# Performance work log

Measured on AMD Instinct MI355X. Metric: run time of the kernel, lower is better.

## Reference

```python
import jax, jax.numpy as jnp
import numpy as np

N_HEADS = 16
N_EMBD = 1024

def setup_inputs() -> dict:
    key = jax.random.key(0)
    k1, k2, k3, k4, k5 = jax.random.split(key, 5)
    B, T, C = 4, 2048, N_EMBD
    x = jax.random.normal(k1, (B, T, C), dtype=jnp.float32)
    # Linear weights stored as [in, out] (equivalent math to torch's x @ W.T + b)
    W_attn = jax.random.normal(k2, (C, 3 * C), dtype=jnp.float32) * 0.02
    b_attn = jax.random.normal(k3, (3 * C,), dtype=jnp.float32) * 0.02
    W_proj = jax.random.normal(k4, (C, C), dtype=jnp.float32) * 0.02
    b_proj = jax.random.normal(k5, (C,), dtype=jnp.float32) * 0.02
    return {"x": x, "W_attn": W_attn, "b_attn": b_attn, "W_proj": W_proj, "b_proj": b_proj}

def reference(x, W_attn, b_attn, W_proj, b_proj):
    B, T, C = x.shape
    H = N_HEADS
    D = C // H
    scale = 1.0 / jnp.sqrt(jnp.asarray(D, dtype=x.dtype))
    # fused QKV projection
    qkv = x @ W_attn + b_attn                      # [B, T, 3C]
    q, k, v = jnp.split(qkv, 3, axis=-1)           # each [B, T, C]
    q = q.reshape(B, T, H, D)
    k = k.reshape(B, T, H, D)
    v = v.reshape(B, T, H, D)
    # non-causal SDPA
    scores = jnp.einsum('bqhd,bkhd->bhqk', q, k) * scale  # [B, H, T, T]
    attn = jax.nn.softmax(scores, axis=-1)
    y = jnp.einsum('bhqk,bkhd->bqhd', attn, v)     # [B, T, H, D]
    y = y.reshape(B, T, C)
    return y @ W_proj + b_proj
```

## Files before the change

### kernel.cpp

```cpp
#include <hip/hip_runtime.h>

typedef short s16x8 __attribute__((ext_vector_type(8)));
typedef short s16x4 __attribute__((ext_vector_type(4)));
typedef float f32x4 __attribute__((ext_vector_type(4)));
typedef float f32x16 __attribute__((ext_vector_type(16)));

__device__ __forceinline__ unsigned short f2bf(float f) {
  unsigned u = __float_as_uint(f);
  u += 0x7fffu + ((u >> 16) & 1u);
  return (unsigned short)(u >> 16);
}
__device__ __forceinline__ float bf2f(unsigned short h) {
  return __uint_as_float(((unsigned)h) << 16);
}

#define GLOAD_LDS16(g, l)                                          \
  __builtin_amdgcn_global_load_lds(                                \
      (const __attribute__((address_space(1))) void*)(g),          \
      (__attribute__((address_space(3))) void*)(l), 16, 0, 0)


__global__ __launch_bounds__(256) void cvt_x_bf16(const float* __restrict__ in,
                                                  unsigned short* __restrict__ out) {
  int i = (blockIdx.x * 256 + threadIdx.x) * 4;
  float4 v = *(const float4*)(in + i);
  ushort4 o;
  o.x = f2bf(v.x); o.y = f2bf(v.y); o.z = f2bf(v.z); o.w = f2bf(v.w);
  *(ushort4*)(out + i) = o;
}

__global__ __launch_bounds__(256) void transpose_w(const float* __restrict__ W,
                                                   unsigned short* __restrict__ Wt,
                                                   int R, int C) {
  __shared__ float tile[32][33];
  int c0 = blockIdx.x * 32, r0 = blockIdx.y * 32;
  int x = threadIdx.x, ty = threadIdx.y;
  for (int yy = ty; yy < 32; yy += 8)
    tile[yy][x] = W[(size_t)(r0 + yy) * C + c0 + x];
  __syncthreads();
  for (int yy = ty; yy < 32; yy += 8)
    Wt[(size_t)(c0 + yy) * R + r0 + x] = f2bf(tile[x][yy]);
}

__global__ __launch_bounds__(256) void transpose_v(const unsigned short* __restrict__ qkv,
                                                   unsigned short* __restrict__ vt) {
  __shared__ unsigned short TT[32][72];
  const int bh = blockIdx.y;
  const int t0 = blockIdx.x * 32;
  const int b = bh >> 4, h = bh & 15;
  const int t = threadIdx.x;
  {
    int row = t >> 3, c8 = (t & 7) * 8;
    const unsigned short* src =
        qkv + (size_t)(b * 2048 + t0 + row) * 3072 + 2048 + h * 64 + c8;
    *(uint4*)&TT[row][c8] = *(const uint4*)src;
  }
  __syncthreads();
  {
    int drow = t >> 2, tc8 = (t & 3) * 8;
    uint4 val;
    unsigned short* vp = (unsigned short*)&val;
    for (int j = 0; j < 8; j++) vp[j] = TT[tc8 + j][drow];
    *(uint4*)(vt + (size_t)(bh * 64 + drow) * 2048 + t0 + tc8) = val;
  }
}


template <bool OUT_BF16>
__global__ __launch_bounds__(256) void gemm_bt(const unsigned short* __restrict__ A,
                                               const unsigned short* __restrict__ Bt,
                                               const float* __restrict__ bias,
                                               void* __restrict__ Cout,
                                               int M, int N, int K) {
  __shared__ __align__(16) unsigned short As[2][128 * 32];
  __shared__ __align__(16) unsigned short Bs[2][128 * 32];

  const int tid  = threadIdx.x;
  const int lane = tid & 63;
  const int w    = tid >> 6;
  const int lm   = lane & 31;
  const int l5   = lane >> 5;
  const int wm   = (w >> 1) * 64;
  const int wn   = (w & 1) * 64;
  const int m0   = blockIdx.x * 128;
  const int n0   = blockIdx.y * 128;

  f32x16 acc[2][2];
  for (int i = 0; i < 2; i++)
    for (int j = 0; j < 2; j++)
      for (int r = 0; r < 16; r++) acc[i][j][r] = 0.f;

  const int srow = tid >> 2;
  const int scb  = (((tid & 3) ^ ((srow >> 1) & 3)) * 8);
  const unsigned short* Ap = A  + (size_t)(m0 + srow) * K + scb;
  const unsigned short* Bp = Bt + (size_t)(n0 + srow) * K + scb;

#define STAGE_G(bb, kk)                                                  \
  do {                                                                   \
    GLOAD_LDS16(Ap + (kk), &As[bb][w * 512]);                            \
    GLOAD_LDS16(Ap + (size_t)64 * K + (kk), &As[bb][2048 + w * 512]);    \
    GLOAD_LDS16(Bp + (kk), &Bs[bb][w * 512]);                            \
    GLOAD_LDS16(Bp + (size_t)64 * K + (kk), &Bs[bb][2048 + w * 512]);    \
  } while (0)

  const int rx = ((lm >> 1) & 3) << 4;

  STAGE_G(0, 0);
  int cur = 0;
  for (int kk = 0; kk < K; kk += 32) {
    __syncthreads();
    if (kk + 32 < K) STAGE_G(cur ^ 1, kk + 32);

    const char* Ab = (const char*)As[cur];
    const char* Bb = (const char*)Bs[cur];
    s16x8 af[2][2], bfr[2][2];
    for (int i = 0; i < 2; i++)
      for (int ks = 0; ks < 2; ks++)
        af[i][ks] = *(const s16x8*)(Ab + (wm + i * 32 + lm) * 64 +
                                    (((l5 * 16 + ks * 32)) ^ rx));
    for (int j = 0; j < 2; j++)
      for (int ks = 0; ks < 2; ks++)
        bfr[j][ks] = *(const s16x8*)(Bb + (wn + j * 32 + lm) * 64 +
                                     (((l5 * 16 + ks * 32)) ^ rx));
    for (int ks = 0; ks < 2; ks++)
      for (int i = 0; i < 2; i++)
        for (int j = 0; j < 2; j++)
          acc[i][j] = __builtin_amdgcn_mfma_f32_32x32x16_bf16(af[i][ks], bfr[j][ks],
                                                              acc[i][j], 0, 0, 0);
    cur ^= 1;
  }
#undef STAGE_G

  for (int j = 0; j < 2; j++) {
    int col = n0 + wn + j * 32 + lm;
    float bc = bias[col];
    for (int i = 0; i < 2; i++) {
      int rowb = m0 + wm + i * 32 + l5 * 4;
      for (int r = 0; r < 16; r++) {
        int row = rowb + (r & 3) + 8 * (r >> 2);
        float v = acc[i][j][r] + bc;
        if (OUT_BF16)
          ((unsigned short*)Cout)[(size_t)row * N + col] = f2bf(v);
        else
          ((float*)Cout)[(size_t)row * N + col] = v;
      }
    }
  }
}


__global__ __launch_bounds__(256, 4) void attn_flash(const unsigned short* __restrict__ qkv,
                                                     const unsigned short* __restrict__ vt,
                                                     unsigned short* __restrict__ y) {
  const int T = 2048, C3 = 3072;
  const int bh = blockIdx.x & 63;
  const int qt = blockIdx.x >> 6;
  const int b  = bh >> 4;
  const int h  = bh & 15;
  const int q0 = qt * 128;

  const int tid  = threadIdx.x;
  const int lane = tid & 63;
  const int w    = tid >> 6;
  const int lr   = lane & 15;
  const int quad = lane >> 4;

  __shared__ __align__(16) unsigned short Ks[2][64][64];
  __shared__ __align__(16) unsigned short Vs[2][64][64];

  s16x8 qf[2][2];
  const float QSC = 0.18033688f;
  for (int j = 0; j < 2; j++)
    for (int c = 0; c < 2; c++) {
      const unsigned short* qp =
          qkv + (size_t)(b * T + q0 + w * 32 + j * 16 + lr) * C3 + h * 64 + c * 32 + quad * 8;
      s16x8 t = *(const s16x8*)qp;
      s16x8 o;
      for (int e = 0; e < 8; e++)
        o[e] = (short)f2bf(bf2f((unsigned short)t[e]) * QSC);
      qf[j][c] = o;
    }

  s16x8 ones;
  for (int e = 0; e < 8; e++) ones[e] = (short)0x3F80;

  f32x4 O[2][4];
  f32x4 Lacc[2];
  for (int j = 0; j < 2; j++) {
    for (int dt = 0; dt < 4; dt++) O[j][dt] = f32x4{0.f, 0.f, 0.f, 0.f};
    Lacc[j] = f32x4{0.f, 0.f, 0.f, 0.f};
  }

  const int srow = tid >> 3;
  const int scol = (((tid & 7) ^ (srow & 7)) * 8);
  const int kperm = (((srow & 12) << 1) | ((srow >> 4) << 2) | (srow & 3));

  const unsigned short* kbase = qkv + (size_t)(b * T) * C3 + 1024 + (size_t)h * 64;
  const unsigned short* vbase = vt + (size_t)(bh * 64) * 2048;
  const unsigned short* kp0 = kbase + (size_t)(kperm)      * C3 + scol;
  const unsigned short* kp1 = kbase + (size_t)(32 + kperm) * C3 + scol;
  const unsigned short* vp0 = vbase + (size_t)(srow)      * 2048 + scol;
  const unsigned short* vp1 = vbase + (size_t)(srow + 32) * 2048 + scol;

#define STAGE_KV(bb, k0off)                                                  \
  do {                                                                       \
    GLOAD_LDS16(kp0 + (size_t)(k0off) * C3, &Ks[bb][w * 8][0]);              \
    GLOAD_LDS16(kp1 + (size_t)(k0off) * C3, &Ks[bb][w * 8 + 32][0]);         \
    GLOAD_LDS16(vp0 + (k0off), &Vs[bb][w * 8][0]);                           \
    GLOAD_LDS16(vp1 + (k0off), &Vs[bb][w * 8 + 32][0]);                      \
  } while (0)

  const int rswz = (lr & 7) << 4;

  STAGE_KV(0, 0);
  int cur = 0;
  for (int kt = 0; kt < 32; kt++) {
    __syncthreads();
    if (kt < 31) STAGE_KV(cur ^ 1, (kt + 1) * 64);

    const char* KsB = (const char*)&Ks[cur][0][0];
    const char* VsB = (const char*)&Vs[cur][0][0];

    for (int ch = 0; ch < 2; ch++) {
      const char* krowA = KsB + (ch * 32 + lr) * 128;
      const char* krowB = KsB + (ch * 32 + 16 + lr) * 128;
      s16x8 kA0 = *(const s16x8*)(krowA + ((quad * 16) ^ rswz));
      s16x8 kA1 = *(const s16x8*)(krowA + ((64 + quad * 16) ^ rswz));
      s16x8 kB0 = *(const s16x8*)(krowB + ((quad * 16) ^ rswz));
      s16x8 kB1 = *(const s16x8*)(krowB + ((64 + quad * 16) ^ rswz));
      s16x8 vf[4];
      for (int dt = 0; dt < 4; dt++)
        vf[dt] = *(const s16x8*)(VsB + (dt * 16 + lr) * 128 + ((ch * 64 + quad * 16) ^ rswz));

      for (int j = 0; j < 2; j++) {
        f32x4 Sa = f32x4{0.f, 0.f, 0.f, 0.f};
        f32x4 Sb = f32x4{0.f, 0.f, 0.f, 0.f};
        Sa = __builtin_amdgcn_mfma_f32_16x16x32_bf16(kA0, qf[j][0], Sa, 0, 0, 0);
        Sa = __builtin_amdgcn_mfma_f32_16x16x32_bf16(kA1, qf[j][1], Sa, 0, 0, 0);
        Sb = __builtin_amdgcn_mfma_f32_16x16x32_bf16(kB0, qf[j][0], Sb, 0, 0, 0);
        Sb = __builtin_amdgcn_mfma_f32_16x16x32_bf16(kB1, qf[j][1], Sb, 0, 0, 0);
        unsigned u0 = __float_as_uint(__builtin_amdgcn_exp2f(Sa[0])) + 0x8000u;
        unsigned u1 = __float_as_uint(__builtin_amdgcn_exp2f(Sa[1])) + 0x8000u;
        unsigned u2 = __float_as_uint(__builtin_amdgcn_exp2f(Sa[2])) + 0x8000u;
        unsigned u3 = __float_as_uint(__builtin_amdgcn_exp2f(Sa[3])) + 0x8000u;
        unsigned u4 = __float_as_uint(__builtin_amdgcn_exp2f(Sb[0])) + 0x8000u;
        unsigned u5 = __float_as_uint(__builtin_amdgcn_exp2f(Sb[1])) + 0x8000u;
        unsigned u6 = __float_as_uint(__builtin_amdgcn_exp2f(Sb[2])) + 0x8000u;
        unsigned u7 = __float_as_uint(__builtin_amdgcn_exp2f(Sb[3])) + 0x8000u;
        union { unsigned u[4]; s16x8 v; } pk;
        pk.u[0] = __builtin_amdgcn_perm(u1, u0, 0x07060302u);
        pk.u[1] = __builtin_amdgcn_perm(u3, u2, 0x07060302u);
        pk.u[2] = __builtin_amdgcn_perm(u5, u4, 0x07060302u);
        pk.u[3] = __builtin_amdgcn_perm(u7, u6, 0x07060302u);
        Lacc[j] = __builtin_amdgcn_mfma_f32_16x16x32_bf16(pk.v, ones, Lacc[j], 0, 0, 0);
        for (int dt = 0; dt < 4; dt++)
          O[j][dt] = __builtin_amdgcn_mfma_f32_16x16x32_bf16(pk.v, vf[dt], O[j][dt], 0, 0, 0);
      }
    }
    cur ^= 1;
  }
#undef STAGE_KV

  for (int j = 0; j < 2; j++) {
    for (int r = 0; r < 4; r++) {
      float inv = 1.f / Lacc[j][r];
      int row = b * T + q0 + w * 32 + j * 16 + quad * 4 + r;
      for (int dt = 0; dt < 4; dt++) {
        int col = h * 64 + dt * 16 + lr;
        y[(size_t)row * 1024 + col] = f2bf(O[j][dt][r] * inv);
      }
    }
  }
}


extern "C" void kernel_launch(void* const* d_in, const int* in_sizes, int n_in,
                              void* d_out, int out_size, void* d_ws, size_t ws_size,
                              hipStream_t stream) {
  const float* x  = (const float*)d_in[0];
  const float* Wa = (const float*)d_in[1];
  const float* ba = (const float*)d_in[2];
  const float* Wp = (const float*)d_in[3];
  const float* bp = (const float*)d_in[4];
  float* out = (float*)d_out;

  char* ws = (char*)d_ws;
  unsigned short* xb  = (unsigned short*)ws;
  unsigned short* Wat = (unsigned short*)(ws + 16777216);
  unsigned short* Wpt = (unsigned short*)(ws + 23068672);
  unsigned short* qkv = (unsigned short*)(ws + 25165824);
  unsigned short* vtr = (unsigned short*)(ws + 75497472);

  cvt_x_bf16<<<8192, 256, 0, stream>>>(x, xb);
  transpose_w<<<dim3(96, 32), dim3(32, 8), 0, stream>>>(Wa, Wat, 1024, 3072);
  transpose_w<<<dim3(32, 32), dim3(32, 8), 0, stream>>>(Wp, Wpt, 1024, 1024);

  gemm_bt<true><<<dim3(64, 24), 256, 0, stream>>>(xb, Wat, ba, qkv, 8192, 3072, 1024);

  transpose_v<<<dim3(64, 64), 256, 0, stream>>>(qkv, vtr);

  attn_flash<<<1024, 256, 0, stream>>>(qkv, vtr, xb);

  gemm_bt<false><<<dim3(64, 8), 256, 0, stream>>>(xb, Wpt, bp, out, 8192, 1024, 1024);
}
```

Baseline: 277.6 us.

## Fuse V transpose into QKV GEMM epilogue and unroll attention loop

The QKV GEMM now writes the V block directly in transposed [b,h,d,t] layout from its epilogue, which removes the separate transpose_v kernel and its extra read and write of V. The attention main loop is unrolled by two with fixed buffer indices and pointer increments. It also adds s_setprio around MFMA groups and uses the hardware packed bf16 convert in place of manual rounding. The V stores are now 8-byte strided writes along t, which may coalesce less well than the row-major writes they replace.

```diff
diff --git a/kernel.cpp b/kernel.cpp
--- a/kernel.cpp
+++ b/kernel.cpp
@@ -42,35 +42,13 @@
     Wt[(size_t)(c0 + yy) * R + r0 + x] = f2bf(tile[x][yy]);
 }
 
-__global__ __launch_bounds__(256) void transpose_v(const unsigned short* __restrict__ qkv,
-                                                   unsigned short* __restrict__ vt) {
-  __shared__ unsigned short TT[32][72];
-  const int bh = blockIdx.y;
-  const int t0 = blockIdx.x * 32;
-  const int b = bh >> 4, h = bh & 15;
-  const int t = threadIdx.x;
-  {
-    int row = t >> 3, c8 = (t & 7) * 8;
-    const unsigned short* src =
-        qkv + (size_t)(b * 2048 + t0 + row) * 3072 + 2048 + h * 64 + c8;
-    *(uint4*)&TT[row][c8] = *(const uint4*)src;
-  }
-  __syncthreads();
-  {
-    int drow = t >> 2, tc8 = (t & 3) * 8;
-    uint4 val;
-    unsigned short* vp = (unsigned short*)&val;
-    for (int j = 0; j < 8; j++) vp[j] = TT[tc8 + j][drow];
-    *(uint4*)(vt + (size_t)(bh * 64 + drow) * 2048 + t0 + tc8) = val;
-  }
-}
-
-
-template <bool OUT_BF16>
+
+template <int MODE>
 __global__ __launch_bounds__(256) void gemm_bt(const unsigned short* __restrict__ A,
                                                const unsigned short* __restrict__ Bt,
                                                const float* __restrict__ bias,
                                                void* __restrict__ Cout,
+                                               unsigned short* __restrict__ vtr,
                                                int M, int N, int K) {
   __shared__ __align__(16) unsigned short As[2][128 * 32];
   __shared__ __align__(16) unsigned short Bs[2][128 * 32];
@@ -131,18 +109,38 @@
   }
 #undef STAGE_G
 
-  for (int j = 0; j < 2; j++) {
-    int col = n0 + wn + j * 32 + lm;
-    float bc = bias[col];
-    for (int i = 0; i < 2; i++) {
-      int rowb = m0 + wm + i * 32 + l5 * 4;
-      for (int r = 0; r < 16; r++) {
-        int row = rowb + (r & 3) + 8 * (r >> 2);
-        float v = acc[i][j][r] + bc;
-        if (OUT_BF16)
-          ((unsigned short*)Cout)[(size_t)row * N + col] = f2bf(v);
-        else
-          ((float*)Cout)[(size_t)row * N + col] = v;
+  if (MODE == 1 && n0 >= 2048) {
+    const int bidx = m0 >> 11;
+    for (int j = 0; j < 2; j++) {
+      int col = n0 + wn + j * 32 + lm;
+      float bc = bias[col];
+      size_t vrow = (size_t)((bidx << 10) + (col - 2048)) * 2048;
+      for (int i = 0; i < 2; i++) {
+        int tb = (m0 & 2047) + wm + i * 32 + l5 * 4;
+        for (int g = 0; g < 4; g++) {
+          ushort4 o;
+          o.x = f2bf(acc[i][j][g * 4 + 0] + bc);
+          o.y = f2bf(acc[i][j][g * 4 + 1] + bc);
+          o.z = f2bf(acc[i][j][g * 4 + 2] + bc);
+          o.w = f2bf(acc[i][j][g * 4 + 3] + bc);
+          *(ushort4*)(vtr + vrow + tb + 8 * g) = o;
+        }
+      }
+    }
+  } else {
+    for (int j = 0; j < 2; j++) {
+      int col = n0 + wn + j * 32 + lm;
+      float bc = bias[col];
+      for (int i = 0; i < 2; i++) {
+        int rowb = m0 + wm + i * 32 + l5 * 4;
+        for (int r = 0; r < 16; r++) {
+          int row = rowb + (r & 3) + 8 * (r >> 2);
+          float v = acc[i][j][r] + bc;
+          if (MODE == 1)
+            ((unsigned short*)Cout)[(size_t)row * N + col] = f2bf(v);
+          else
+            ((float*)Cout)[(size_t)row * N + col] = v;
+        }
       }
     }
   }
@@ -202,64 +200,77 @@
   const unsigned short* vp0 = vbase + (size_t)(srow)      * 2048 + scol;
   const unsigned short* vp1 = vbase + (size_t)(srow + 32) * 2048 + scol;
 
-#define STAGE_KV(bb, k0off)                                                  \
+#define STAGE_KV(bb)                                                         \
   do {                                                                       \
-    GLOAD_LDS16(kp0 + (size_t)(k0off) * C3, &Ks[bb][w * 8][0]);              \
-    GLOAD_LDS16(kp1 + (size_t)(k0off) * C3, &Ks[bb][w * 8 + 32][0]);         \
-    GLOAD_LDS16(vp0 + (k0off), &Vs[bb][w * 8][0]);                           \
-    GLOAD_LDS16(vp1 + (k0off), &Vs[bb][w * 8 + 32][0]);                      \
+    GLOAD_LDS16(kp0, &Ks[bb][w * 8][0]);                                     \
+    GLOAD_LDS16(kp1, &Ks[bb][w * 8 + 32][0]);                                \
+    GLOAD_LDS16(vp0, &Vs[bb][w * 8][0]);                                     \
+    GLOAD_LDS16(vp1, &Vs[bb][w * 8 + 32][0]);                                \
+    kp0 += (size_t)64 * C3; kp1 += (size_t)64 * C3;                          \
+    vp0 += 64; vp1 += 64;                                                    \
   } while (0)
 
   const int rswz = (lr & 7) << 4;
 
-  STAGE_KV(0, 0);
-  int cur = 0;
-  for (int kt = 0; kt < 32; kt++) {
+#define COMPUTE(bb)                                                              \
+  do {                                                                           \
+    const char* KsB = (const char*)&Ks[bb][0][0];                                \
+    const char* VsB = (const char*)&Vs[bb][0][0];                                \
+    for (int ch = 0; ch < 2; ch++) {                                             \
+      const char* krowA = KsB + (ch * 32 + lr) * 128;                            \
+      const char* krowB = KsB + (ch * 32 + 16 + lr) * 128;                       \
+      s16x8 kA0 = *(const s16x8*)(krowA + ((quad * 16) ^ rswz));                 \
+      s16x8 kA1 = *(const s16x8*)(krowA + ((64 + quad * 16) ^ rswz));            \
+      s16x8 kB0 = *(const s16x8*)(krowB + ((quad * 16) ^ rswz));                 \
+      s16x8 kB1 = *(const s16x8*)(krowB + ((64 + quad * 16) ^ rswz));            \
+      s16x8 vf[4];                                                               \
+      for (int dt = 0; dt < 4; dt++)                                             \
+        vf[dt] = *(const s16x8*)(VsB + (dt * 16 + lr) * 128 +                    \
+                                 ((ch * 64 + quad * 16) ^ rswz));                \
+      for (int j = 0; j < 2; j++) {                                              \
+        f32x4 Sa = f32x4{0.f, 0.f, 0.f, 0.f};                                    \
+        f32x4 Sb = f32x4{0.f, 0.f, 0.f, 0.f};                                    \
+        __builtin_amdgcn_s_setprio(1);                                           \
+        Sa = __builtin_amdgcn_mfma_f32_16x16x32_bf16(kA0, qf[j][0], Sa, 0, 0, 0);\
+        Sa = __builtin_amdgcn_mfma_f32_16x16x32_bf16(kA1, qf[j][1], Sa, 0, 0, 0);\
+        Sb = __builtin_amdgcn_mfma_f32_16x16x32_bf16(kB0, qf[j][0], Sb, 0, 0, 0);\
+        Sb = __builtin_amdgcn_mfma_f32_16x16x32_bf16(kB1, qf[j][1], Sb, 0, 0, 0);\
+        __builtin_amdgcn_s_setprio(0);                                           \
+        float p0 = __builtin_amdgcn_exp2f(Sa[0]);                                \
+        float p1 = __builtin_amdgcn_exp2f(Sa[1]);                                \
+        float p2 = __builtin_amdgcn_exp2f(Sa[2]);                                \
+        float p3 = __builtin_amdgcn_exp2f(Sa[3]);                                \
+        float p4 = __builtin_amdgcn_exp2f(Sb[0]);                                \
+        float p5 = __builtin_amdgcn_exp2f(Sb[1]);                                \
+        float p6 = __builtin_amdgcn_exp2f(Sb[2]);                                \
+        float p7 = __builtin_amdgcn_exp2f(Sb[3]);                                \
+        union { unsigned u[4]; s16x8 v; } pk;                                    \
+        asm("v_cvt_pk_bf16_f32 %0, %1, %2" : "=v"(pk.u[0]) : "v"(p0), "v"(p1));  \
+        asm("v_cvt_pk_bf16_f32 %0, %1, %2" : "=v"(pk.u[1]) : "v"(p2), "v"(p3));  \
+        asm("v_cvt_pk_bf16_f32 %0, %1, %2" : "=v"(pk.u[2]) : "v"(p4), "v"(p5));  \
+        asm("v_cvt_pk_bf16_f32 %0, %1, %2" : "=v"(pk.u[3]) : "v"(p6), "v"(p7));  \
+        __builtin_amdgcn_s_setprio(1);                                           \
+        Lacc[j] = __builtin_amdgcn_mfma_f32_16x16x32_bf16(pk.v, ones, Lacc[j],   \
+                                                          0, 0, 0);              \
+        for (int dt = 0; dt < 4; dt++)                                           \
+          O[j][dt] = __builtin_amdgcn_mfma_f32_16x16x32_bf16(pk.v, vf[dt],       \
+                                                             O[j][dt], 0, 0, 0); \
+        __builtin_amdgcn_s_setprio(0);                                           \
+      }                                                                          \
+    }                                                                            \
+  } while (0)
+
+  STAGE_KV(0);
+  for (int kt2 = 0; kt2 < 16; kt2++) {
     __syncthreads();
-    if (kt < 31) STAGE_KV(cur ^ 1, (kt + 1) * 64);
-
-    const char* KsB = (const char*)&Ks[cur][0][0];
-    const char* VsB = (const char*)&Vs[cur][0][0];
-
-    for (int ch = 0; ch < 2; ch++) {
-      const char* krowA = KsB + (ch * 32 + lr) * 128;
-      const char* krowB = KsB + (ch * 32 + 16 + lr) * 128;
-      s16x8 kA0 = *(const s16x8*)(krowA + ((quad * 16) ^ rswz));
-      s16x8 kA1 = *(const s16x8*)(krowA + ((64 + quad * 16) ^ rswz));
-      s16x8 kB0 = *(const s16x8*)(krowB + ((quad * 16) ^ rswz));
-      s16x8 kB1 = *(const s16x8*)(krowB + ((64 + quad * 16) ^ rswz));
-      s16x8 vf[4];
-      for (int dt = 0; dt < 4; dt++)
-        vf[dt] = *(const s16x8*)(VsB + (dt * 16 + lr) * 128 + ((ch * 64 + quad * 16) ^ rswz));
-
-      for (int j = 0; j < 2; j++) {
-        f32x4 Sa = f32x4{0.f, 0.f, 0.f, 0.f};
-        f32x4 Sb = f32x4{0.f, 0.f, 0.f, 0.f};
-        Sa = __builtin_amdgcn_mfma_f32_16x16x32_bf16(kA0, qf[j][0], Sa, 0, 0, 0);
-        Sa = __builtin_amdgcn_mfma_f32_16x16x32_bf16(kA1, qf[j][1], Sa, 0, 0, 0);
-        Sb = __builtin_amdgcn_mfma_f32_16x16x32_bf16(kB0, qf[j][0], Sb, 0, 0, 0);
-        Sb = __builtin_amdgcn_mfma_f32_16x16x32_bf16(kB1, qf[j][1], Sb, 0, 0, 0);
-        unsigned u0 = __float_as_uint(__builtin_amdgcn_exp2f(Sa[0])) + 0x8000u;
-        unsigned u1 = __float_as_uint(__builtin_amdgcn_exp2f(Sa[1])) + 0x8000u;
-        unsigned u2 = __float_as_uint(__builtin_amdgcn_exp2f(Sa[2])) + 0x8000u;
-        unsigned u3 = __float_as_uint(__builtin_amdgcn_exp2f(Sa[3])) + 0x8000u;
-        unsigned u4 = __float_as_uint(__builtin_amdgcn_exp2f(Sb[0])) + 0x8000u;
-        unsigned u5 = __float_as_uint(__builtin_amdgcn_exp2f(Sb[1])) + 0x8000u;
-        unsigned u6 = __float_as_uint(__builtin_amdgcn_exp2f(Sb[2])) + 0x8000u;
-        unsigned u7 = __float_as_uint(__builtin_amdgcn_exp2f(Sb[3])) + 0x8000u;
-        union { unsigned u[4]; s16x8 v; } pk;
-        pk.u[0] = __builtin_amdgcn_perm(u1, u0, 0x07060302u);
-        pk.u[1] = __builtin_amdgcn_perm(u3, u2, 0x07060302u);
-        pk.u[2] = __builtin_amdgcn_perm(u5, u4, 0x07060302u);
-        pk.u[3] = __builtin_amdgcn_perm(u7, u6, 0x07060302u);
-        Lacc[j] = __builtin_amdgcn_mfma_f32_16x16x32_bf16(pk.v, ones, Lacc[j], 0, 0, 0);
-        for (int dt = 0; dt < 4; dt++)
-          O[j][dt] = __builtin_amdgcn_mfma_f32_16x16x32_bf16(pk.v, vf[dt], O[j][dt], 0, 0, 0);
-      }
-    }
-    cur ^= 1;
+    STAGE_KV(1);
+    COMPUTE(0);
+    __syncthreads();
+    if (kt2 < 15) STAGE_KV(0);
+    COMPUTE(1);
   }
 #undef STAGE_KV
+#undef COMPUTE
 
   for (int j = 0; j < 2; j++) {
     for (int r = 0; r < 4; r++) {
@@ -295,11 +306,9 @@
   transpose_w<<<dim3(96, 32), dim3(32, 8), 0, stream>>>(Wa, Wat, 1024, 3072);
   transpose_w<<<dim3(32, 32), dim3(32, 8), 0, stream>>>(Wp, Wpt, 1024, 1024);
 
-  gemm_bt<true><<<dim3(64, 24), 256, 0, stream>>>(xb, Wat, ba, qkv, 8192, 3072, 1024);
-
-  transpose_v<<<dim3(64, 64), 256, 0, stream>>>(qkv, vtr);
+  gemm_bt<1><<<dim3(64, 24), 256, 0, stream>>>(xb, Wat, ba, qkv, vtr, 8192, 3072, 1024);
 
   attn_flash<<<1024, 256, 0, stream>>>(qkv, vtr, xb);
 
-  gemm_bt<false><<<dim3(64, 8), 256, 0, stream>>>(xb, Wpt, bp, out, 8192, 1024, 1024);
-}
+  gemm_bt<0><<<dim3(64, 8), 256, 0, stream>>>(xb, Wpt, bp, out, nullptr, 8192, 1024, 1024);
+}
```

New measurement: 269.8 us. -2.8%, faster.
